# Performance work log

Measured on AMD Instinct MI355X. Metric: run time of the kernel, lower is better.

## Reference

```python
import jax, jax.numpy as jnp
import numpy as np

B, DX, DZ, DY = 8192, 512, 1024, 256


def setup_inputs() -> dict:
    key = jax.random.key(0)
    ks = jax.random.split(key, 13)
    s = 0.02
    return {
        "xs": jax.random.normal(ks[0], (B, DX), dtype=jnp.float32),
        "Wx": jax.random.normal(ks[1], (DZ, DX), dtype=jnp.float32) * s,
        "bx": jnp.zeros((DZ,), dtype=jnp.float32),
        "Wy": jax.random.normal(ks[2], (DZ, DY), dtype=jnp.float32) * s,
        "by": jnp.zeros((DZ,), dtype=jnp.float32),
        "Wn": jax.random.normal(ks[3], (DZ, 3 * DZ), dtype=jnp.float32) * s,
        "bn": jnp.zeros((DZ,), dtype=jnp.float32),
        "Wu": jax.random.normal(ks[4], (DY, DZ), dtype=jnp.float32) * s,
        "bu": jnp.zeros((DY,), dtype=jnp.float32),
        "Wq": jax.random.normal(ks[5], (DY, DZ), dtype=jnp.float32) * s,
        "bq": jnp.zeros((DY,), dtype=jnp.float32),
        "ys_init": jax.random.normal(ks[6], (B, DY), dtype=jnp.float32),
        "zs_init": jax.random.normal(ks[7], (B, DZ), dtype=jnp.float32),
        "T": 4,
        "n": 6,
    }


def reference(xs, Wx, bx, Wy, by, Wn, bn, Wu, bu, Wq, bq, ys_init, zs_init, T, n):
    xs_e = xs @ Wx.T + bx                      # [B, DZ]
    ys_e = ys_init @ Wy.T + by                 # [B, DZ]
    zs = zs_init                               # [B, DZ]
    null = jnp.zeros_like(xs_e)

    def query(x, y, z):
        w = jnp.concatenate([x, y, z], axis=-1)  # [B, 3*DZ]
        return jnp.tanh(w @ Wn.T + bn)

    # no-grad refinement (T-1 outer iterations)
    for _ in range(T - 1):
        for _ in range(n):
            zs = query(xs_e, ys_e, zs)
        ys_e = query(null, ys_e, zs)
    ys_e = jax.lax.stop_gradient(ys_e)
    zs = jax.lax.stop_gradient(zs)

    # final grad-enabled block
    for _ in range(n):
        zs = query(xs_e, ys_e, zs)
    ys_e = query(null, ys_e, zs)

    y_hat = jax.nn.sigmoid(ys_e @ Wu.T + bu)
    q_hat = jax.nn.sigmoid(ys_e @ Wq.T + bq)
    return (y_hat, q_hat)
```

## Files before the change

kernel.cpp:

```cpp
#include <hip/hip_runtime.h>
#include <hip/hip_bf16.h>
#include <cstdint>
#include <cstddef>

#define B_   8192
#define DX_  512
#define DZ_  1024
#define DY_  256
#define T_   4
#define NN_  6

typedef float f32x4 __attribute__((ext_vector_type(4)));
typedef short s16x8 __attribute__((ext_vector_type(8)));
typedef __hip_bfloat16 bf16;

__device__ __forceinline__ void gload_lds16(const bf16* g, void* l) {
  __builtin_amdgcn_global_load_lds(
      (const __attribute__((address_space(1))) void*)g,
      (__attribute__((address_space(3))) void*)l,
      16, 0, 0);
}

__device__ __forceinline__ float bf2f(unsigned short u) {
  union { unsigned int i; float f; } cv; cv.i = ((unsigned int)u) << 16; return cv.f;
}

__global__ void cvt_bf16_kernel(const float* __restrict__ in, bf16* __restrict__ out, int n4) {
  int i = blockIdx.x * blockDim.x + threadIdx.x;
  if (i >= n4) return;
  float4 v = ((const float4*)in)[i];
  ushort4 o;
  bf16 a0 = __float2bfloat16(v.x); o.x = *(unsigned short*)&a0;
  bf16 a1 = __float2bfloat16(v.y); o.y = *(unsigned short*)&a1;
  bf16 a2 = __float2bfloat16(v.z); o.z = *(unsigned short*)&a2;
  bf16 a3 = __float2bfloat16(v.w); o.w = *(unsigned short*)&a3;
  ((ushort4*)out)[i] = o;
}

__global__ void pack_bias_kernel(const float* __restrict__ a, const float* __restrict__ b,
                                 float* __restrict__ o) {
  int i = threadIdx.x;
  o[i] = (i < DY_) ? a[i] : b[i - DY_];
}

template<int ACT, int MODE, bool HASADD>
__global__ __launch_bounds__(512, 2)
void gemm_bt(const bf16* __restrict__ A, int lda,
             const bf16* __restrict__ W, int ldw,
             const float* __restrict__ bias,
             const bf16* __restrict__ add1,
             bf16* __restrict__ out_pre,
             void* __restrict__ out, void* __restrict__ out2,
             int N, int K)
{
  __shared__ __align__(16) char ldsc[4 * 24576];
  const int t    = threadIdx.x;
  const int lane = t & 63;
  const int wave = t >> 6;
  const int m0 = blockIdx.x * 128;
  const int n0 = blockIdx.y * 256;

  const int rowA = t >> 2;
  const int q    = (t & 3) ^ ((t >> 3) & 3);
  const bf16* gA  = A + (size_t)(m0 + rowA) * lda + q * 8;
  const bf16* gB1 = W + (size_t)(n0 + rowA) * ldw + q * 8;
  const bf16* gB2 = gB1 + (size_t)128 * ldw;
  const int wb = wave * 1024;

  auto stage = [&](int ko, int buf) {
    char* base = ldsc + buf * 24576;
    gload_lds16(gA + ko, base + wb);
    gload_lds16(gB1 + ko, base + 8192 + wb);
    gload_lds16(gB2 + ko, base + 16384 + wb);
  };

  const int mo = (wave >> 2) * 64;
  const int no = (wave & 3) * 64;
  const int fr = lane & 15;
  const int g4 = lane >> 4;
  const int rb = g4 * 4;
  const int kx = (g4 ^ ((fr >> 1) & 3)) * 16;

  float bv[4] = {0.f, 0.f, 0.f, 0.f};
  if (bias) {
#pragma unroll
    for (int j = 0; j < 4; ++j) bv[j] = bias[n0 + no + j * 16 + fr];
  }
  unsigned short adr[4][4][4];
  if (HASADD) {
#pragma unroll
    for (int f = 0; f < 4; ++f)
#pragma unroll
      for (int j = 0; j < 4; ++j) {
        const unsigned short* p = (const unsigned short*)add1
            + (size_t)(m0 + mo + f * 16 + rb) * N + (n0 + no + j * 16 + fr);
#pragma unroll
        for (int r = 0; r < 4; ++r) adr[f][j][r] = p[(size_t)r * N];
      }
  }
  __builtin_amdgcn_sched_barrier(0);
  stage(0, 0);
  stage(32, 1);
  stage(64, 2);
  __builtin_amdgcn_sched_barrier(0);

  f32x4 acc[4][4];
#pragma unroll
  for (int f = 0; f < 4; ++f)
#pragma unroll
    for (int j = 0; j < 4; ++j)
#pragma unroll
      for (int r = 0; r < 4; ++r) {
        float v = bv[j];
        if (HASADD && MODE != 1) v += bf2f(adr[f][j][r]);
        acc[f][j][r] = v;
      }

  s16x8 aA[4], bA[4], aB[4], bB[4];
  auto ldfrags = [&](int kt, s16x8* fa, s16x8* fb) {
    const char* pA = ldsc + (kt & 3) * 24576;
    const char* pB = pA + 8192;
#pragma unroll
    for (int f = 0; f < 4; ++f) fa[f] = *(const s16x8*)(pA + (mo + f * 16 + fr) * 64 + kx);
#pragma unroll
    for (int j = 0; j < 4; ++j) fb[j] = *(const s16x8*)(pB + (no + j * 16 + fr) * 64 + kx);
  };
  auto domfma = [&](const s16x8* fa, const s16x8* fb) {
    __builtin_amdgcn_s_setprio(1);
#pragma unroll
    for (int f = 0; f < 4; ++f)
#pragma unroll
      for (int j = 0; j < 4; ++j)
        acc[f][j] = __builtin_amdgcn_mfma_f32_16x16x32_bf16(fa[f], fb[j], acc[f][j], 0, 0, 0);
    __builtin_amdgcn_s_setprio(0);
  };

  const int NT = K >> 5;

  asm volatile("s_waitcnt vmcnt(6)" ::: "memory");
  __builtin_amdgcn_s_barrier();
  __builtin_amdgcn_sched_barrier(0);
  ldfrags(0, aA, bA);

  for (int kt = 0; kt < NT; kt += 2) {
    if (kt + 2 < NT) asm volatile("s_waitcnt vmcnt(3)" ::: "memory");
    else             asm volatile("s_waitcnt vmcnt(0)" ::: "memory");
    __builtin_amdgcn_s_barrier();
    __builtin_amdgcn_sched_barrier(0);
    if (kt + 3 < NT) stage((kt + 3) << 5, (kt + 3) & 3);
    ldfrags(kt + 1, aB, bB);
    domfma(aA, bA);
    if (kt + 2 < NT) {
      if (kt + 3 < NT) asm volatile("s_waitcnt vmcnt(3)" ::: "memory");
      else             asm volatile("s_waitcnt vmcnt(0)" ::: "memory");
      __builtin_amdgcn_s_barrier();
      __builtin_amdgcn_sched_barrier(0);
      if (kt + 4 < NT) stage((kt + 4) << 5, (kt + 4) & 3);
      ldfrags(kt + 2, aA, bA);
    }
    domfma(aB, bB);
  }

#pragma unroll
  for (int f = 0; f < 4; ++f) {
#pragma unroll
    for (int j = 0; j < 4; ++j) {
      const int n = n0 + no + j * 16 + fr;
#pragma unroll
      for (int r = 0; r < 4; ++r) {
        const int m = m0 + mo + f * 16 + rb + r;
        float v = acc[f][j][r];
        if (MODE == 1) {
          out_pre[(size_t)m * N + n] = __float2bfloat16(v);
          v += bf2f(adr[f][j][r]);
        }
        if (ACT == 1)      { float e = __expf(2.f * v); v = 1.f - 2.f / (e + 1.f); }
        else if (ACT == 2) v = 1.f / (1.f + __expf(-v));
        if (MODE == 2) {
          if (n < DY_) ((float*)out)[(size_t)m * DY_ + n] = v;
          else         ((float*)out2)[(size_t)m * DY_ + (n - DY_)] = v;
        } else {
          ((bf16*)out)[(size_t)m * N + n] = __float2bfloat16(v);
        }
      }
    }
  }
}

extern "C" void kernel_launch(void* const* d_in, const int* in_sizes, int n_in,
                              void* d_out, int out_size, void* d_ws, size_t ws_size,
                              hipStream_t stream) {
  const float* xs  = (const float*)d_in[0];
  const float* Wx  = (const float*)d_in[1];
  const float* bx  = (const float*)d_in[2];
  const float* Wy  = (const float*)d_in[3];
  const float* by  = (const float*)d_in[4];
  const float* Wn  = (const float*)d_in[5];
  const float* bn  = (const float*)d_in[6];
  const float* Wu  = (const float*)d_in[7];
  const float* bu  = (const float*)d_in[8];
  const float* Wq  = (const float*)d_in[9];
  const float* bq  = (const float*)d_in[10];
  const float* ys0 = (const float*)d_in[11];
  const float* zs0 = (const float*)d_in[12];

  char* ws = (char*)d_ws;
  size_t off = 0;
  auto take = [&](size_t bytes) -> char* {
    char* p = ws + off;
    off += (bytes + 255) & ~(size_t)255;
    return p;
  };

  bf16*  Wn_b  = (bf16*)take((size_t)DZ_ * 3 * DZ_ * 2);
  bf16*  Wx_b  = (bf16*)take((size_t)DZ_ * DX_ * 2);
  bf16*  Wy_b  = (bf16*)take((size_t)DZ_ * DY_ * 2);
  bf16*  Wuq_b = (bf16*)take((size_t)2 * DY_ * DZ_ * 2);
  float* buq   = (float*)take((size_t)2 * DY_ * 4);
  bf16*  ys_b  = (bf16*)take((size_t)B_ * DZ_ * 2);
  bf16*  z_a   = (bf16*)take((size_t)B_ * DZ_ * 2);
  bf16*  z_b   = (bf16*)take((size_t)B_ * DZ_ * 2);
  bf16*  cx    = (bf16*)take((size_t)B_ * DZ_ * 2);
  bf16*  cy    = (bf16*)take((size_t)B_ * DZ_ * 2);
  bf16*  c     = (bf16*)take((size_t)B_ * DZ_ * 2);
  bf16* xs_b   = c;
  bf16* ysin_b = (bf16*)((char*)c + (size_t)B_ * DX_ * 2);
  bf16* xse_b  = cy;

  auto cvt = [&](const float* src, bf16* dst, size_t n) {
    int n4 = (int)(n / 4);
    cvt_bf16_kernel<<<(n4 + 255) / 256, 256, 0, stream>>>(src, dst, n4);
  };
  cvt(Wn, Wn_b, (size_t)DZ_ * 3 * DZ_);
  cvt(Wx, Wx_b, (size_t)DZ_ * DX_);
  cvt(Wy, Wy_b, (size_t)DZ_ * DY_);
  cvt(Wu, Wuq_b, (size_t)DY_ * DZ_);
  cvt(Wq, Wuq_b + (size_t)DY_ * DZ_, (size_t)DY_ * DZ_);
  cvt(xs, xs_b, (size_t)B_ * DX_);
  cvt(ys0, ysin_b, (size_t)B_ * DY_);
  cvt(zs0, z_a, (size_t)B_ * DZ_);
  pack_bias_kernel<<<1, 512, 0, stream>>>(bu, bq, buq);

  const dim3 blk(512);
  const dim3 gz(B_ / 128, DZ_ / 256);
  const dim3 gh(B_ / 128, 2);

  gemm_bt<0, 0, false><<<gz, blk, 0, stream>>>(xs_b, DX_, Wx_b, DX_, bx, nullptr, nullptr, xse_b, nullptr, DZ_, DX_);
  gemm_bt<0, 0, false><<<gz, blk, 0, stream>>>(ysin_b, DY_, Wy_b, DY_, by, nullptr, nullptr, ys_b, nullptr, DZ_, DY_);
  gemm_bt<0, 0, false><<<gz, blk, 0, stream>>>(xse_b, DZ_, Wn_b, 3 * DZ_, nullptr, nullptr, nullptr, cx, nullptr, DZ_, DZ_);

  bf16* zc = z_a;
  bf16* zn = z_b;
  for (int tt = 0; tt < T_; ++tt) {
    gemm_bt<0, 1, true><<<gz, blk, 0, stream>>>(ys_b, DZ_, Wn_b + DZ_, 3 * DZ_, bn, cx, cy, c, nullptr, DZ_, DZ_);
    for (int i = 0; i < NN_; ++i) {
      gemm_bt<1, 0, true><<<gz, blk, 0, stream>>>(zc, DZ_, Wn_b + 2 * DZ_, 3 * DZ_, nullptr, c, nullptr, zn, nullptr, DZ_, DZ_);
      bf16* tmp = zc; zc = zn; zn = tmp;
    }
    gemm_bt<1, 0, true><<<gz, blk, 0, stream>>>(zc, DZ_, Wn_b + 2 * DZ_, 3 * DZ_, nullptr, cy, nullptr, ys_b, nullptr, DZ_, DZ_);
  }

  float* outp = (float*)d_out;
  gemm_bt<2, 2, false><<<gh, blk, 0, stream>>>(ys_b, DZ_, Wuq_b, DZ_, buq, nullptr, nullptr,
                                               outp, outp + (size_t)B_ * DY_, 2 * DY_, DZ_);
}
```

Before: 984.1 us.

## Retile GEMM to 256x128 blocks with K=64 stages and triple buffering

The GEMM block tile changes from 128x256 to 256x128, and the K step per stage grows from 32 to 64. The staging buffers go from four buffers with three stages in flight to three 48KB buffers with a two-stage prefetch, using a wider XOR swizzle over 8 chunks. Each stage is split into two MFMA half-steps with barriers between them. The MODE==1 residual add now reads directly from global memory in the epilogue instead of being preloaded into registers, which frees registers. The larger LDS footprint (144KB) may limit occupancy to one block per CU despite launch_bounds(512,2), and fewer, longer K iterations reduce barrier overhead.

Measured after the change: 941.8 us. 1.04x faster.

```diff
diff --git a/kernel.cpp b/kernel.cpp
--- a/kernel.cpp
+++ b/kernel.cpp
@@ -53,33 +53,37 @@
              void* __restrict__ out, void* __restrict__ out2,
              int N, int K)
 {
-  __shared__ __align__(16) char ldsc[4 * 24576];
+  __shared__ __align__(16) char ldsc[3 * 49152];
   const int t    = threadIdx.x;
   const int lane = t & 63;
   const int wave = t >> 6;
-  const int m0 = blockIdx.x * 128;
-  const int n0 = blockIdx.y * 256;
-
-  const int rowA = t >> 2;
-  const int q    = (t & 3) ^ ((t >> 3) & 3);
-  const bf16* gA  = A + (size_t)(m0 + rowA) * lda + q * 8;
-  const bf16* gB1 = W + (size_t)(n0 + rowA) * ldw + q * 8;
-  const bf16* gB2 = gB1 + (size_t)128 * ldw;
+  const int m0 = blockIdx.x * 256;
+  const int n0 = blockIdx.y * 128;
+
+  const int srow = t >> 3;
+  const int q    = (t & 7) ^ ((t >> 3) & 7);
+  const bf16* gA = A + (size_t)(m0 + srow) * lda + q * 8;
+  const bf16* gB = W + (size_t)(n0 + srow) * ldw + q * 8;
   const int wb = wave * 1024;
 
-  auto stage = [&](int ko, int buf) {
-    char* base = ldsc + buf * 24576;
-    gload_lds16(gA + ko, base + wb);
-    gload_lds16(gB1 + ko, base + 8192 + wb);
-    gload_lds16(gB2 + ko, base + 16384 + wb);
-  };
-
-  const int mo = (wave >> 2) * 64;
-  const int no = (wave & 3) * 64;
+  auto stage = [&](int kt) {
+    char* base = ldsc + (kt % 3) * 49152;
+    const int ko = kt << 6;
+#pragma unroll
+    for (int i = 0; i < 4; ++i)
+      gload_lds16(gA + (size_t)(i * 64) * lda + ko, base + i * 8192 + wb);
+#pragma unroll
+    for (int i = 0; i < 2; ++i)
+      gload_lds16(gB + (size_t)(i * 64) * ldw + ko, base + 32768 + i * 8192 + wb);
+  };
+
+  const int mo = (wave >> 1) * 64;
+  const int no = (wave & 1) * 64;
   const int fr = lane & 15;
   const int g4 = lane >> 4;
   const int rb = g4 * 4;
-  const int kx = (g4 ^ ((fr >> 1) & 3)) * 16;
+
+  const int NT = K >> 6;
 
   float bv[4] = {0.f, 0.f, 0.f, 0.f};
   if (bias) {
@@ -87,7 +91,7 @@
     for (int j = 0; j < 4; ++j) bv[j] = bias[n0 + no + j * 16 + fr];
   }
   unsigned short adr[4][4][4];
-  if (HASADD) {
+  if (HASADD && MODE != 1) {
 #pragma unroll
     for (int f = 0; f < 4; ++f)
 #pragma unroll
@@ -99,9 +103,8 @@
       }
   }
   __builtin_amdgcn_sched_barrier(0);
-  stage(0, 0);
-  stage(32, 1);
-  stage(64, 2);
+  stage(0);
+  stage(1);
   __builtin_amdgcn_sched_barrier(0);
 
   f32x4 acc[4][4];
@@ -116,14 +119,15 @@
         acc[f][j][r] = v;
       }
 
-  s16x8 aA[4], bA[4], aB[4], bB[4];
-  auto ldfrags = [&](int kt, s16x8* fa, s16x8* fb) {
-    const char* pA = ldsc + (kt & 3) * 24576;
-    const char* pB = pA + 8192;
-#pragma unroll
-    for (int f = 0; f < 4; ++f) fa[f] = *(const s16x8*)(pA + (mo + f * 16 + fr) * 64 + kx);
-#pragma unroll
-    for (int j = 0; j < 4; ++j) fb[j] = *(const s16x8*)(pB + (no + j * 16 + fr) * 64 + kx);
+  s16x8 a0[4], b0[4], a1[4], b1[4];
+  auto ldfrags = [&](int kt, int s, s16x8* fa, s16x8* fb) {
+    const char* pA = ldsc + (kt % 3) * 49152;
+    const char* pB = pA + 32768;
+    const int cb = ((s * 4 + g4) ^ (fr & 7)) * 16;
+#pragma unroll
+    for (int f = 0; f < 4; ++f) fa[f] = *(const s16x8*)(pA + (mo + f * 16 + fr) * 128 + cb);
+#pragma unroll
+    for (int j = 0; j < 4; ++j) fb[j] = *(const s16x8*)(pB + (no + j * 16 + fr) * 128 + cb);
   };
   auto domfma = [&](const s16x8* fa, const s16x8* fb) {
     __builtin_amdgcn_s_setprio(1);
@@ -135,30 +139,25 @@
     __builtin_amdgcn_s_setprio(0);
   };
 
-  const int NT = K >> 5;
-
   asm volatile("s_waitcnt vmcnt(6)" ::: "memory");
   __builtin_amdgcn_s_barrier();
-  __builtin_amdgcn_sched_barrier(0);
-  ldfrags(0, aA, bA);
-
-  for (int kt = 0; kt < NT; kt += 2) {
-    if (kt + 2 < NT) asm volatile("s_waitcnt vmcnt(3)" ::: "memory");
+
+  for (int kt = 0; kt < NT; ++kt) {
+    ldfrags(kt, 0, a0, b0);
+    __builtin_amdgcn_sched_barrier(0);
+    __builtin_amdgcn_s_barrier();
+    asm volatile("s_waitcnt lgkmcnt(0)" ::: "memory");
+    __builtin_amdgcn_sched_barrier(0);
+    domfma(a0, b0);
+    ldfrags(kt, 1, a1, b1);
+    if (kt + 2 < NT) stage(kt + 2);
+    __builtin_amdgcn_sched_barrier(0);
+    if (kt + 2 < NT) asm volatile("s_waitcnt vmcnt(6)" ::: "memory");
     else             asm volatile("s_waitcnt vmcnt(0)" ::: "memory");
     __builtin_amdgcn_s_barrier();
-    __builtin_amdgcn_sched_barrier(0);
-    if (kt + 3 < NT) stage((kt + 3) << 5, (kt + 3) & 3);
-    ldfrags(kt + 1, aB, bB);
-    domfma(aA, bA);
-    if (kt + 2 < NT) {
-      if (kt + 3 < NT) asm volatile("s_waitcnt vmcnt(3)" ::: "memory");
-      else             asm volatile("s_waitcnt vmcnt(0)" ::: "memory");
-      __builtin_amdgcn_s_barrier();
-      __builtin_amdgcn_sched_barrier(0);
-      if (kt + 4 < NT) stage((kt + 4) << 5, (kt + 4) & 3);
-      ldfrags(kt + 2, aA, bA);
-    }
-    domfma(aB, bB);
+    asm volatile("s_waitcnt lgkmcnt(0)" ::: "memory");
+    __builtin_amdgcn_sched_barrier(0);
+    domfma(a1, b1);
   }
 
 #pragma unroll
@@ -172,7 +171,7 @@
         float v = acc[f][j][r];
         if (MODE == 1) {
           out_pre[(size_t)m * N + n] = __float2bfloat16(v);
-          v += bf2f(adr[f][j][r]);
+          v += bf2f(((const unsigned short*)add1)[(size_t)m * N + n]);
         }
         if (ACT == 1)      { float e = __expf(2.f * v); v = 1.f - 2.f / (e + 1.f); }
         else if (ACT == 2) v = 1.f / (1.f + __expf(-v));
@@ -242,8 +241,8 @@
   pack_bias_kernel<<<1, 512, 0, stream>>>(bu, bq, buq);
 
   const dim3 blk(512);
-  const dim3 gz(B_ / 128, DZ_ / 256);
-  const dim3 gh(B_ / 128, 2);
+  const dim3 gz(B_ / 256, DZ_ / 128);
+  const dim3 gh(B_ / 256, 4);
 
   gemm_bt<0, 0, false><<<gz, blk, 0, stream>>>(xs_b, DX_, Wx_b, DX_, bx, nullptr, nullptr, xse_b, nullptr, DZ_, DX_);
   gemm_bt<0, 0, false><<<gz, blk, 0, stream>>>(ysin_b, DY_, Wy_b, DY_, by, nullptr, nullptr, ys_b, nullptr, DZ_, DY_);
```
